# Kernel tuning notes

Hardware: AMD Instinct MI355X
Metric: run time of the kernel (lower is better)

## Reference

```python
import jax, jax.numpy as jnp
import numpy as np

B, T, C = 2, 2048, 2048
H, HD = 16, 128          # n_head, head_dim
LORA = C // 4            # kv_lora_rank = n_embd // compression_ratio
RD = HD // 2             # qk_rope_dim
ND = HD - RD             # qk_nope_dim
THETA = 100000.0


def setup_inputs() -> dict:
    key = jax.random.key(0)
    k0, k1, k2, k3, k4 = jax.random.split(key, 5)
    s = 0.02
    return {
        "x": jax.random.normal(k0, (B, T, C), dtype=jnp.float32),
        "Wq": jax.random.normal(k1, (C, H * HD), dtype=jnp.float32) * s,
        "Wkva": jax.random.normal(k2, (C, LORA + RD), dtype=jnp.float32) * s,
        "Wkvb": jax.random.normal(k3, (LORA, H * ND), dtype=jnp.float32) * s,
        "Wo": jax.random.normal(k4, (H * HD, C), dtype=jnp.float32) * s,
    }


def apply_rope(x, theta=THETA):
    # x: [B, H, T, D] with D even; interleaved complex rotation (torch.view_as_complex style)
    b, h, t, d = x.shape
    freqs = 1.0 / (theta ** (jnp.arange(0, d, 2, dtype=jnp.float32) / d))  # [D/2]
    ang = jnp.arange(t, dtype=jnp.float32)[:, None] * freqs[None, :]       # [T, D/2]
    cos, sin = jnp.cos(ang), jnp.sin(ang)
    xr = x.reshape(b, h, t, d // 2, 2)
    x0, x1 = xr[..., 0], xr[..., 1]
    o0 = x0 * cos - x1 * sin
    o1 = x0 * sin + x1 * cos
    return jnp.stack([o0, o1], axis=-1).reshape(b, h, t, d)


def reference(x, Wq, Wkva, Wkvb, Wo):
    Bx, Tx, Cx = x.shape
    # query projection -> [B, H, T, HD]
    q = (x @ Wq).reshape(Bx, Tx, H, HD).transpose(0, 2, 1, 3)
    # compressed KV + shared (MQA) rope key
    ckv = x @ Wkva                                  # [B, T, LORA+RD]
    kv_latent = ckv[..., :LORA]                     # [B, T, LORA]
    k_rope = ckv[..., LORA:]                        # [B, T, RD]
    # decompress nope part of K (== nope part of V)
    kv = (kv_latent @ Wkvb).reshape(Bx, Tx, H, ND).transpose(0, 2, 1, 3)  # [B,H,T,ND]
    k_rope = jnp.broadcast_to(k_rope[:, None, :, :], (Bx, H, Tx, RD))
    q_nope, q_rope = q[..., :ND], q[..., ND:]
    q_rope = apply_rope(q_rope)
    k_rope = apply_rope(k_rope)
    qf = jnp.concatenate([q_nope, q_rope], axis=-1)               # [B,H,T,HD]
    kf = jnp.concatenate([kv, k_rope], axis=-1)                   # [B,H,T,HD]
    vf = jnp.concatenate([kv, jnp.zeros_like(k_rope)], axis=-1)   # [B,H,T,HD]
    scale = 1.0 / np.sqrt(HD).astype(np.float32)
    att = jnp.einsum("bhtd,bhsd->bhts", qf, kf) * scale           # [B,H,T,T]
    causal = jnp.tril(jnp.ones((Tx, Tx), dtype=bool))
    att = jnp.where(causal, att, -jnp.inf)
    att = jax.nn.softmax(att, axis=-1)
    y = jnp.einsum("bhts,bhsd->bhtd", att, vf)                    # [B,H,T,HD]
    y = y.transpose(0, 2, 1, 3).reshape(Bx, Tx, H * HD)
    return y @ Wo
```

## Files before the change

kernel.cpp:

```cpp
#include <hip/hip_runtime.h>
#include <hip/hip_bf16.h>
#include <math.h>

#define B_ 2
#define T_ 2048
#define C_ 2048
#define H_ 16
#define HD_ 128
#define LORA_ 512
#define RD_ 64
#define ND_ 64
#define BT_ (B_*T_)
#define NKVA_ 576
#define NKVAP_ 640
#define LOG2_THETA 16.609640474436812f

typedef __bf16 bf16x8 __attribute__((ext_vector_type(8)));
typedef float  f32x4  __attribute__((ext_vector_type(4)));

#define MFMA16(a,b,c) __builtin_amdgcn_mfma_f32_16x16x32_bf16((a),(b),(c),0,0,0)

__device__ static inline void load_lds16(const __bf16* g, __bf16* l) {
  auto* lp = (__attribute__((address_space(3))) char*)(uintptr_t)(l);
  auto* gp = (const __attribute__((address_space(1))) char*)(g);
  __builtin_amdgcn_global_load_lds(gp, lp, 16, 0, 0);
}

__device__ static inline unsigned pkbf(float a, float b) {
  union { __bf16 h[2]; unsigned u; } v;
  v.h[0] = (__bf16)a; v.h[1] = (__bf16)b;
  return v.u;
}

__global__ __launch_bounds__(256) void k_cast_x(const float* __restrict__ x,
                                                __bf16* __restrict__ xb, int n) {
  int idx = blockIdx.x * 256 + threadIdx.x;
  if (idx < n) xb[idx] = (__bf16)x[idx];
}

__global__ __launch_bounds__(256) void k_tcast(const float* __restrict__ src,
                                               __bf16* __restrict__ dst,
                                               int K, int N, int NP) {
  __shared__ float tile[32][33];
  int k0 = blockIdx.x * 32;
  int n0 = blockIdx.y * 32;
  int tx = threadIdx.x & 31, ty = threadIdx.x >> 5;
  for (int i = ty; i < 32; i += 8) {
    int n = n0 + tx;
    tile[i][tx] = (n < N) ? src[(size_t)(k0 + i) * N + n] : 0.0f;
  }
  __syncthreads();
  for (int i = ty; i < 32; i += 8) {
    dst[(size_t)(n0 + i) * K + k0 + tx] = (__bf16)tile[tx][i];
  }
}

__global__ __launch_bounds__(256) void k_tcast_wo(const float* __restrict__ Wo,
                                                  __bf16* __restrict__ dst) {
  __shared__ float tile[32][33];
  int kc0 = blockIdx.x * 32;
  int n0  = blockIdx.y * 32;
  int rbase = (kc0 >> 6) * 128 + (kc0 & 63);
  int tx = threadIdx.x & 31, ty = threadIdx.x >> 5;
  for (int i = ty; i < 32; i += 8)
    tile[i][tx] = Wo[(size_t)(rbase + i) * C_ + n0 + tx];
  __syncthreads();
  for (int i = ty; i < 32; i += 8)
    dst[(size_t)(n0 + i) * 1024 + kc0 + tx] = (__bf16)tile[tx][i];
}

__global__ __launch_bounds__(256) void k_gemm_bt(const __bf16* __restrict__ A,
                                                 const __bf16* __restrict__ B,
                                                 float* __restrict__ C,
                                                 int M, int N, int K) {
  __shared__ __align__(16) __bf16 As[2][128 * 32];
  __shared__ __align__(16) __bf16 Bs[2][128 * 32];
  const int tid  = threadIdx.x;
  const int lane = tid & 63;
  const int wave = tid >> 6;
  const int bm = blockIdx.x, bn = blockIdx.y;
  const int r0 = tid >> 2;
  const int c8 = (tid & 3) * 8;
  const __bf16* Ag = A + (size_t)(bm * 128 + r0) * K + c8;
  const __bf16* Bg = B + (size_t)(bn * 128 + r0) * K + c8;
  const int wr = (wave >> 1) * 64, wc = (wave & 1) * 64;
  const int fr = lane & 15, fk = (lane >> 4) * 8;
  const f32x4 fzero = {0.f, 0.f, 0.f, 0.f};
  f32x4 acc[4][4];
#pragma unroll
  for (int i = 0; i < 4; ++i)
#pragma unroll
    for (int j = 0; j < 4; ++j) acc[i][j] = fzero;

  load_lds16(Ag,                  &As[0][tid * 8]);
  load_lds16(Ag + (size_t)64 * K, &As[0][tid * 8 + 2048]);
  load_lds16(Bg,                  &Bs[0][tid * 8]);
  load_lds16(Bg + (size_t)64 * K, &Bs[0][tid * 8 + 2048]);

  int buf = 0;
  for (int k0 = 0; k0 < K; k0 += 32) {
    __syncthreads();
    if (k0 + 32 < K) {
      const int nb = buf ^ 1;
      load_lds16(Ag + k0 + 32,                  &As[nb][tid * 8]);
      load_lds16(Ag + (size_t)64 * K + k0 + 32, &As[nb][tid * 8 + 2048]);
      load_lds16(Bg + k0 + 32,                  &Bs[nb][tid * 8]);
      load_lds16(Bg + (size_t)64 * K + k0 + 32, &Bs[nb][tid * 8 + 2048]);
    }
    bf16x8 af[4], bfg[4];
#pragma unroll
    for (int i = 0; i < 4; ++i) af[i]  = *(const bf16x8*)&As[buf][(wr + i * 16 + fr) * 32 + fk];
#pragma unroll
    for (int j = 0; j < 4; ++j) bfg[j] = *(const bf16x8*)&Bs[buf][(wc + j * 16 + fr) * 32 + fk];
#pragma unroll
    for (int i = 0; i < 4; ++i)
#pragma unroll
      for (int j = 0; j < 4; ++j)
        acc[i][j] = MFMA16(af[i], bfg[j], acc[i][j]);
    buf ^= 1;
  }
  const int rbase = (lane >> 4) * 4;
  float* Cb = C + (size_t)(bm * 128 + wr + rbase) * N + bn * 128 + wc + fr;
#pragma unroll
  for (int i = 0; i < 4; ++i)
#pragma unroll
    for (int j = 0; j < 4; ++j)
#pragma unroll
      for (int r = 0; r < 4; ++r)
        Cb[(size_t)(i * 16 + r) * N + j * 16] = acc[i][j][r];
}

__global__ __launch_bounds__(256) void k_rope_q(const float* __restrict__ q,
                                                __bf16* __restrict__ qf) {
  const float scale2 = 1.4426950408889634f / 11.313708498984760f;
  int idx = blockIdx.x * 256 + threadIdx.x;
  int d  = idx & 127;
  int t  = (idx >> 7) & 2047;
  int bh = idx >> 18;
  int h  = bh & 15, b = bh >> 4;
  const float* qrow = q + ((size_t)(b * T_ + t)) * 2048 + h * 128;
  float v;
  if (d < 64) {
    v = qrow[d];
  } else {
    int i = (d - 64) >> 1;
    float freq = exp2f(-((float)(2 * i) / 64.0f) * LOG2_THETA);
    float ang = (float)t * freq;
    float c = cosf(ang), s = sinf(ang);
    float x0 = qrow[64 + 2 * i], x1 = qrow[64 + 2 * i + 1];
    v = (d & 1) ? (x0 * s + x1 * c) : (x0 * c - x1 * s);
  }
  qf[idx] = (__bf16)(v * scale2);
}

__global__ __launch_bounds__(256) void k_rope_kf(const float* __restrict__ ckv,
                                                 __bf16* __restrict__ kf) {
  int idx = blockIdx.x * 256 + threadIdx.x;
  int d = idx & 63;
  int t = (idx >> 6) & 2047;
  int h = (idx >> 17) & 15;
  int b = idx >> 21;
  const float* src = ckv + ((size_t)(b * T_ + t)) * NKVAP_ + 512;
  int i = d >> 1;
  float freq = exp2f(-((float)(2 * i) / 64.0f) * LOG2_THETA);
  float ang = (float)t * freq;
  float c = cosf(ang), s = sinf(ang);
  float x0 = src[2 * i], x1 = src[2 * i + 1];
  float v = (d & 1) ? (x0 * s + x1 * c) : (x0 * c - x1 * s);
  kf[(((size_t)(b * H_ + h)) * T_ + t) * 128 + 64 + d] = (__bf16)v;
}

__global__ __launch_bounds__(256) void k_cast_kvl(const float* __restrict__ ckv,
                                                  __bf16* __restrict__ kvl) {
  int idx = blockIdx.x * 256 + threadIdx.x;
  int r = idx >> 9, c = idx & 511;
  kvl[idx] = (__bf16)ckv[(size_t)r * NKVAP_ + c];
}

__global__ __launch_bounds__(256) void k_pack_kv(const float* __restrict__ kv,
                                                 __bf16* __restrict__ kf,
                                                 __bf16* __restrict__ kvT) {
  __shared__ float tile[64][65];
  const int bh = blockIdx.x;
  const int b = bh >> 4, h = bh & 15;
  const int t0 = blockIdx.y * 64;
  const int tid = threadIdx.x;
  const int i0 = tid >> 4, d4 = (tid & 15) * 4;
#pragma unroll
  for (int p = 0; p < 4; ++p) {
    int i = i0 + p * 16;
    const float* src = kv + ((size_t)(b * T_ + t0 + i)) * 1024 + h * 64 + d4;
    float4 v = *(const float4*)src;
    tile[i][d4] = v.x; tile[i][d4 + 1] = v.y; tile[i][d4 + 2] = v.z; tile[i][d4 + 3] = v.w;
    union { __bf16 hh[4]; uint2 u; } o;
    o.hh[0] = (__bf16)v.x; o.hh[1] = (__bf16)v.y; o.hh[2] = (__bf16)v.z; o.hh[3] = (__bf16)v.w;
    *(uint2*)(kf + ((size_t)bh * T_ + t0 + i) * 128 + d4) = o.u;
  }
  __syncthreads();
  const int dd = tid >> 2, tc0 = (tid & 3) * 16;
  __bf16 outv[16];
#pragma unroll
  for (int j = 0; j < 16; ++j) outv[j] = (__bf16)tile[tc0 + j][dd];
  __bf16* dst = kvT + ((size_t)(bh * 64 + dd)) * T_ + t0 + tc0;
  *(bf16x8*)dst = *(bf16x8*)&outv[0];
  *(bf16x8*)(dst + 8) = *(bf16x8*)&outv[8];
}

__global__ __launch_bounds__(256, 3) void k_attn(const __bf16* __restrict__ qf,
                                                 const __bf16* __restrict__ kf,
                                                 const __bf16* __restrict__ kvT,
                                                 __bf16* __restrict__ yc) {
  const int blk = blockIdx.x;
  const int bh = blk & 31;
  const int qt = 31 - (blk >> 5);
  const int b = bh >> 4, h = bh & 15;
  const int qbase = qt * 64;
  const int tid = threadIdx.x;
  const int lane = tid & 63, wave = tid >> 6;
  const int fr = lane & 15, quad = lane >> 4, fk8 = quad * 8;

  __shared__ __align__(16) __bf16 Ks[2][64 * 128];
  __shared__ __align__(16) __bf16 Vs[2][64 * 64];

  const int qi = qbase + wave * 16 + fr;
  const __bf16* qb = qf + ((size_t)bh * T_ + qi) * HD_;
  bf16x8 aq[4];
#pragma unroll
  for (int g = 0; g < 4; ++g) aq[g] = *(const bf16x8*)(qb + g * 32 + fk8);

  const f32x4 fzero = {0.f, 0.f, 0.f, 0.f};
  f32x4 accO[4];
#pragma unroll
  for (int g = 0; g < 4; ++g) accO[g] = fzero;
  float m = -1e30f, l = 0.f;

  const int srow = tid >> 4, scolh = (tid & 15) * 8;
  const int vrow = tid >> 3, vcolh = (tid & 7) * 8;
  const int kwcol = scolh ^ ((srow & 7) * 8);
  const int vwcol = vcolh ^ ((vrow & 7) * 8);
  const int kswz = (fr & 7) * 8;
  const __bf16* kbh = kf + (size_t)bh * T_ * 128;
  const __bf16* vbh = kvT + (size_t)bh * 64 * T_;
  const int srcA = (quad & 1) * 32 + fr, srcB = srcA + 16;
  const int hi = quad >> 1;

  bf16x8 kreg[4], vreg[2];
  auto load_regs = [&](int S) {
#pragma unroll
    for (int p = 0; p < 4; ++p)
      kreg[p] = *(const bf16x8*)(kbh + (size_t)(S + srow + p * 16) * 128 + scolh);
#pragma unroll
    for (int p = 0; p < 2; ++p)
      vreg[p] = *(const bf16x8*)(vbh + (size_t)(vrow + p * 32) * T_ + S + vcolh);
  };
  auto write_buf = [&](int bufi) {
#pragma unroll
    for (int p = 0; p < 4; ++p)
      *(bf16x8*)&Ks[bufi][(srow + p * 16) * 128 + kwcol] = kreg[p];
#pragma unroll
    for (int p = 0; p < 2; ++p)
      *(bf16x8*)&Vs[bufi][(vrow + p * 32) * 64 + vwcol] = vreg[p];
  };

  load_regs(0);
  write_buf(0);
  if (qbase > 0) load_regs(64);
  __syncthreads();

  int cur = 0;
  for (int s0 = 0; s0 <= qbase; s0 += 64) {
    if (s0 + 64 <= qbase) write_buf(cur ^ 1);
    if (s0 + 128 <= qbase) load_regs(s0 + 128);

    f32x4 accST[4];
#pragma unroll
    for (int cg = 0; cg < 4; ++cg) accST[cg] = fzero;
    __builtin_amdgcn_s_setprio(1);
#pragma unroll
    for (int cg = 0; cg < 4; ++cg) {
#pragma unroll
      for (int kg = 0; kg < 4; ++kg) {
        bf16x8 bk = *(const bf16x8*)&Ks[cur][(cg * 16 + fr) * 128 + ((kg * 32 + fk8) ^ kswz)];
        accST[cg] = MFMA16(bk, aq[kg], accST[cg]);
      }
    }
    __builtin_amdgcn_s_setprio(0);

    float lmax = -1e30f;
    if (s0 == qbase) {
#pragma unroll
      for (int cg = 0; cg < 4; ++cg) {
#pragma unroll
        for (int r = 0; r < 4; ++r) {
          const int key = s0 + cg * 16 + quad * 4 + r;
          float v = accST[cg][r];
          v = (key <= qi) ? v : -1e30f;
          accST[cg][r] = v;
          lmax = fmaxf(lmax, v);
        }
      }
    } else {
#pragma unroll
      for (int cg = 0; cg < 4; ++cg) {
#pragma unroll
        for (int r = 0; r < 4; ++r) lmax = fmaxf(lmax, accST[cg][r]);
      }
    }
    lmax = fmaxf(lmax, __shfl_xor(lmax, 16, 64));
    lmax = fmaxf(lmax, __shfl_xor(lmax, 32, 64));

    if (!__all(lmax <= m + 8.0f)) {
      const float mn = fmaxf(m, lmax);
      const float alpha = exp2f(m - mn);
      l *= alpha;
#pragma unroll
      for (int g = 0; g < 4; ++g)
#pragma unroll
        for (int r = 0; r < 4; ++r) accO[g][r] *= alpha;
      m = mn;
    }

    float lsum = 0.f;
    unsigned pk0[4], pk1[4];
#pragma unroll
    for (int cg = 0; cg < 4; ++cg) {
      float p0 = exp2f(accST[cg][0] - m);
      float p1 = exp2f(accST[cg][1] - m);
      float p2 = exp2f(accST[cg][2] - m);
      float p3 = exp2f(accST[cg][3] - m);
      lsum += (p0 + p1) + (p2 + p3);
      pk0[cg] = pkbf(p0, p1);
      pk1[cg] = pkbf(p2, p3);
    }
    lsum += __shfl_xor(lsum, 16, 64);
    lsum += __shfl_xor(lsum, 32, 64);
    l += lsum;

#pragma unroll
    for (int ks = 0; ks < 2; ++ks) {
      int a0 = __shfl((int)pk0[2 * ks], srcA, 64);
      int b0 = __shfl((int)pk0[2 * ks + 1], srcA, 64);
      int a1 = __shfl((int)pk1[2 * ks], srcA, 64);
      int b1 = __shfl((int)pk1[2 * ks + 1], srcA, 64);
      int a2 = __shfl((int)pk0[2 * ks], srcB, 64);
      int b2 = __shfl((int)pk0[2 * ks + 1], srcB, 64);
      int a3 = __shfl((int)pk1[2 * ks], srcB, 64);
      int b3 = __shfl((int)pk1[2 * ks + 1], srcB, 64);
      union { int i[4]; bf16x8 v; } pf;
      pf.i[0] = hi ? b0 : a0;
      pf.i[1] = hi ? b1 : a1;
      pf.i[2] = hi ? b2 : a2;
      pf.i[3] = hi ? b3 : a3;
      __builtin_amdgcn_s_setprio(1);
#pragma unroll
      for (int g = 0; g < 4; ++g) {
        bf16x8 vv = *(const bf16x8*)&Vs[cur][(g * 16 + fr) * 64 + ((ks * 32 + fk8) ^ kswz)];
        accO[g] = MFMA16(vv, pf.v, accO[g]);
      }
      __builtin_amdgcn_s_setprio(0);
    }

    __syncthreads();
    cur ^= 1;
  }

  const float linv = 1.0f / l;
  __bf16* yb = yc + ((size_t)(b * T_ + qi)) * 1024 + h * 64 + quad * 4;
#pragma unroll
  for (int g = 0; g < 4; ++g) {
    union { unsigned u[2]; uint2 v; } o;
    o.u[0] = pkbf(accO[g][0] * linv, accO[g][1] * linv);
    o.u[1] = pkbf(accO[g][2] * linv, accO[g][3] * linv);
    *(uint2*)(yb + g * 16) = o.v;
  }
}

extern "C" void kernel_launch(void* const* d_in, const int* in_sizes, int n_in,
                              void* d_out, int out_size, void* d_ws, size_t ws_size,
                              hipStream_t stream) {
  const float* x    = (const float*)d_in[0];
  const float* Wq   = (const float*)d_in[1];
  const float* Wkva = (const float*)d_in[2];
  const float* Wkvb = (const float*)d_in[3];
  const float* Wo   = (const float*)d_in[4];
  float* out = (float*)d_out;
  char* ws = (char*)d_ws;

  size_t off = 0;
  __bf16* xb    = (__bf16*)(ws + off); off += (size_t)BT_ * C_ * 2;
  __bf16* WqT   = (__bf16*)(ws + off); off += (size_t)2048 * 2048 * 2;
  __bf16* WkvaT = (__bf16*)(ws + off); off += (size_t)NKVAP_ * 2048 * 2;
  __bf16* WkvbT = (__bf16*)(ws + off); off += (size_t)1024 * 512 * 2;
  __bf16* WoTc  = (__bf16*)(ws + off); off += (size_t)2048 * 1024 * 2;
  float*  q     = (float*)(ws + off);  off += (size_t)BT_ * 2048 * 4;
  float*  ckv   = (float*)(ws + off);  off += (size_t)BT_ * NKVAP_ * 4;
  __bf16* kvl   = (__bf16*)(ws + off); off += (size_t)BT_ * 512 * 2;
  float*  kv    = (float*)(ws + off);  off += (size_t)BT_ * 1024 * 4;
  __bf16* qfb   = (__bf16*)(ws + off); off += (size_t)B_ * H_ * T_ * HD_ * 2;
  __bf16* yc    = (__bf16*)(ws + off); off += (size_t)BT_ * 1024 * 2;
  __bf16* kfb = (__bf16*)q;
  __bf16* kvT = (__bf16*)((char*)q + (size_t)B_ * H_ * T_ * HD_ * 2);

  k_cast_x<<<(BT_ * C_) / 256, 256, 0, stream>>>(x, xb, BT_ * C_);
  k_tcast<<<dim3(2048 / 32, 2048 / 32), 256, 0, stream>>>(Wq, WqT, 2048, 2048, 2048);
  k_tcast<<<dim3(2048 / 32, NKVAP_ / 32), 256, 0, stream>>>(Wkva, WkvaT, 2048, NKVA_, NKVAP_);
  k_tcast<<<dim3(512 / 32, 1024 / 32), 256, 0, stream>>>(Wkvb, WkvbT, 512, 1024, 1024);
  k_tcast_wo<<<dim3(1024 / 32, 2048 / 32), 256, 0, stream>>>(Wo, WoTc);

  k_gemm_bt<<<dim3(BT_ / 128, 2048 / 128), 256, 0, stream>>>(xb, WqT, q, BT_, 2048, 2048);
  k_gemm_bt<<<dim3(BT_ / 128, NKVAP_ / 128), 256, 0, stream>>>(xb, WkvaT, ckv, BT_, NKVAP_, 2048);

  k_rope_q<<<(B_ * H_ * T_ * HD_) / 256, 256, 0, stream>>>(q, qfb);
  k_cast_kvl<<<(BT_ * 512) / 256, 256, 0, stream>>>(ckv, kvl);

  k_gemm_bt<<<dim3(BT_ / 128, 1024 / 128), 256, 0, stream>>>(kvl, WkvbT, kv, BT_, 1024, 512);
  k_pack_kv<<<dim3(B_ * H_, T_ / 64), 256, 0, stream>>>(kv, kfb, kvT);
  k_rope_kf<<<(B_ * H_ * T_ * 64) / 256, 256, 0, stream>>>(ckv, kfb);

  k_attn<<<(T_ / 64) * B_ * H_, 256, 0, stream>>>(qfb, kfb, kvT, yc);

  k_gemm_bt<<<dim3(BT_ / 128, 2048 / 128), 256, 0, stream>>>(yc, WoTc, out, BT_, 2048, 1024);
}
```

Baseline: 343.5 us.

## Process 128 query rows per attention block, two 16-row tiles per wave

The attention kernel now handles 128 queries per block (32 per wave as two 16-row MFMA tiles), so each K/V tile loaded into LDS is reused across twice as many queries and K/V fragment reads feed two MFMAs. Online softmax state is duplicated per sub-tile, and waves skip key tiles entirely past their causal limit. This halves grid size and raises register pressure (launch bounds lowered to 2 blocks/SIMD), trading occupancy and load balance for reduced K/V traffic.

```diff
diff --git a/kernel.cpp b/kernel.cpp
--- a/kernel.cpp
+++ b/kernel.cpp
@@ -206,15 +206,15 @@
   *(bf16x8*)(dst + 8) = *(bf16x8*)&outv[8];
 }
 
-__global__ __launch_bounds__(256, 3) void k_attn(const __bf16* __restrict__ qf,
+__global__ __launch_bounds__(256, 2) void k_attn(const __bf16* __restrict__ qf,
                                                  const __bf16* __restrict__ kf,
                                                  const __bf16* __restrict__ kvT,
                                                  __bf16* __restrict__ yc) {
   const int blk = blockIdx.x;
   const int bh = blk & 31;
-  const int qt = 31 - (blk >> 5);
+  const int qt = 15 - (blk >> 5);
   const int b = bh >> 4, h = bh & 15;
-  const int qbase = qt * 64;
+  const int qbase = qt * 128;
   const int tid = threadIdx.x;
   const int lane = tid & 63, wave = tid >> 6;
   const int fr = lane & 15, quad = lane >> 4, fk8 = quad * 8;
@@ -222,17 +222,20 @@
   __shared__ __align__(16) __bf16 Ks[2][64 * 128];
   __shared__ __align__(16) __bf16 Vs[2][64 * 64];
 
-  const int qi = qbase + wave * 16 + fr;
-  const __bf16* qb = qf + ((size_t)bh * T_ + qi) * HD_;
-  bf16x8 aq[4];
-#pragma unroll
-  for (int g = 0; g < 4; ++g) aq[g] = *(const bf16x8*)(qb + g * 32 + fk8);
+  const int qw = qbase + wave * 32;
+  bf16x8 aq[2][4];
+#pragma unroll
+  for (int jq = 0; jq < 2; ++jq) {
+    const __bf16* qb = qf + ((size_t)bh * T_ + qw + jq * 16 + fr) * HD_;
+#pragma unroll
+    for (int g = 0; g < 4; ++g) aq[jq][g] = *(const bf16x8*)(qb + g * 32 + fk8);
+  }
 
   const f32x4 fzero = {0.f, 0.f, 0.f, 0.f};
-  f32x4 accO[4];
-#pragma unroll
-  for (int g = 0; g < 4; ++g) accO[g] = fzero;
-  float m = -1e30f, l = 0.f;
+  f32x4 accO[4][2];
+#pragma unroll
+  for (int g = 0; g < 4; ++g) { accO[g][0] = fzero; accO[g][1] = fzero; }
+  float m0 = -1e30f, m1 = -1e30f, l0 = 0.f, l1 = 0.f;
 
   const int srow = tid >> 4, scolh = (tid & 15) * 8;
   const int vrow = tid >> 3, vcolh = (tid & 7) * 8;
@@ -261,117 +264,146 @@
     for (int p = 0; p < 2; ++p)
       *(bf16x8*)&Vs[bufi][(vrow + p * 32) * 64 + vwcol] = vreg[p];
   };
-
+  auto build_pf = [&](const unsigned* pk0, const unsigned* pk1, int ks) {
+    int a0 = __shfl((int)pk0[2 * ks], srcA, 64);
+    int b0 = __shfl((int)pk0[2 * ks + 1], srcA, 64);
+    int a1 = __shfl((int)pk1[2 * ks], srcA, 64);
+    int b1 = __shfl((int)pk1[2 * ks + 1], srcA, 64);
+    int a2 = __shfl((int)pk0[2 * ks], srcB, 64);
+    int b2 = __shfl((int)pk0[2 * ks + 1], srcB, 64);
+    int a3 = __shfl((int)pk1[2 * ks], srcB, 64);
+    int b3 = __shfl((int)pk1[2 * ks + 1], srcB, 64);
+    union { int i[4]; bf16x8 v; } pf;
+    pf.i[0] = hi ? b0 : a0;
+    pf.i[1] = hi ? b1 : a1;
+    pf.i[2] = hi ? b2 : a2;
+    pf.i[3] = hi ? b3 : a3;
+    return pf.v;
+  };
+
+  const int smax = qbase + 64;
   load_regs(0);
   write_buf(0);
-  if (qbase > 0) load_regs(64);
+  load_regs(64);
   __syncthreads();
 
   int cur = 0;
-  for (int s0 = 0; s0 <= qbase; s0 += 64) {
-    if (s0 + 64 <= qbase) write_buf(cur ^ 1);
-    if (s0 + 128 <= qbase) load_regs(s0 + 128);
-
-    f32x4 accST[4];
-#pragma unroll
-    for (int cg = 0; cg < 4; ++cg) accST[cg] = fzero;
-    __builtin_amdgcn_s_setprio(1);
-#pragma unroll
-    for (int cg = 0; cg < 4; ++cg) {
-#pragma unroll
-      for (int kg = 0; kg < 4; ++kg) {
-        bf16x8 bk = *(const bf16x8*)&Ks[cur][(cg * 16 + fr) * 128 + ((kg * 32 + fk8) ^ kswz)];
-        accST[cg] = MFMA16(bk, aq[kg], accST[cg]);
+  for (int s0 = 0; s0 <= smax; s0 += 64) {
+    if (s0 + 64 <= smax) write_buf(cur ^ 1);
+    if (s0 + 128 <= smax) load_regs(s0 + 128);
+
+    if (s0 <= qw + 31) {
+      f32x4 accST[4][2];
+#pragma unroll
+      for (int cg = 0; cg < 4; ++cg) { accST[cg][0] = fzero; accST[cg][1] = fzero; }
+      __builtin_amdgcn_s_setprio(1);
+#pragma unroll
+      for (int cg = 0; cg < 4; ++cg) {
+#pragma unroll
+        for (int kg = 0; kg < 4; ++kg) {
+          bf16x8 bk = *(const bf16x8*)&Ks[cur][(cg * 16 + fr) * 128 + ((kg * 32 + fk8) ^ kswz)];
+          accST[cg][0] = MFMA16(bk, aq[0][kg], accST[cg][0]);
+          accST[cg][1] = MFMA16(bk, aq[1][kg], accST[cg][1]);
+        }
+      }
+      __builtin_amdgcn_s_setprio(0);
+
+      float lmax0 = -1e30f, lmax1 = -1e30f;
+      if (s0 + 63 > qw) {
+        const int qi0 = qw + fr, qi1 = qw + 16 + fr;
+#pragma unroll
+        for (int cg = 0; cg < 4; ++cg) {
+#pragma unroll
+          for (int r = 0; r < 4; ++r) {
+            const int key = s0 + cg * 16 + quad * 4 + r;
+            float v0 = accST[cg][0][r], v1 = accST[cg][1][r];
+            v0 = (key <= qi0) ? v0 : -1e30f;
+            v1 = (key <= qi1) ? v1 : -1e30f;
+            accST[cg][0][r] = v0; accST[cg][1][r] = v1;
+            lmax0 = fmaxf(lmax0, v0); lmax1 = fmaxf(lmax1, v1);
+          }
+        }
+      } else {
+#pragma unroll
+        for (int cg = 0; cg < 4; ++cg) {
+#pragma unroll
+          for (int r = 0; r < 4; ++r) {
+            lmax0 = fmaxf(lmax0, accST[cg][0][r]);
+            lmax1 = fmaxf(lmax1, accST[cg][1][r]);
+          }
+        }
+      }
+      lmax0 = fmaxf(lmax0, __shfl_xor(lmax0, 16, 64));
+      lmax0 = fmaxf(lmax0, __shfl_xor(lmax0, 32, 64));
+      lmax1 = fmaxf(lmax1, __shfl_xor(lmax1, 16, 64));
+      lmax1 = fmaxf(lmax1, __shfl_xor(lmax1, 32, 64));
+
+      if (!__all(lmax0 <= m0 + 8.0f && lmax1 <= m1 + 8.0f)) {
+        const float mn0 = fmaxf(m0, lmax0), mn1 = fmaxf(m1, lmax1);
+        const float al0 = exp2f(m0 - mn0), al1 = exp2f(m1 - mn1);
+        l0 *= al0; l1 *= al1;
+#pragma unroll
+        for (int g = 0; g < 4; ++g) {
+#pragma unroll
+          for (int r = 0; r < 4; ++r) { accO[g][0][r] *= al0; accO[g][1][r] *= al1; }
+        }
+        m0 = mn0; m1 = mn1;
+      }
+
+      float ls0 = 0.f, ls1 = 0.f;
+      unsigned pk0a[4], pk1a[4], pk0b[4], pk1b[4];
+#pragma unroll
+      for (int cg = 0; cg < 4; ++cg) {
+        float p0 = exp2f(accST[cg][0][0] - m0);
+        float p1 = exp2f(accST[cg][0][1] - m0);
+        float p2 = exp2f(accST[cg][0][2] - m0);
+        float p3 = exp2f(accST[cg][0][3] - m0);
+        ls0 += (p0 + p1) + (p2 + p3);
+        pk0a[cg] = pkbf(p0, p1); pk1a[cg] = pkbf(p2, p3);
+        float r0 = exp2f(accST[cg][1][0] - m1);
+        float r1 = exp2f(accST[cg][1][1] - m1);
+        float r2 = exp2f(accST[cg][1][2] - m1);
+        float r3 = exp2f(accST[cg][1][3] - m1);
+        ls1 += (r0 + r1) + (r2 + r3);
+        pk0b[cg] = pkbf(r0, r1); pk1b[cg] = pkbf(r2, r3);
+      }
+      ls0 += __shfl_xor(ls0, 16, 64);
+      ls0 += __shfl_xor(ls0, 32, 64);
+      ls1 += __shfl_xor(ls1, 16, 64);
+      ls1 += __shfl_xor(ls1, 32, 64);
+      l0 += ls0; l1 += ls1;
+
+#pragma unroll
+      for (int ks = 0; ks < 2; ++ks) {
+        bf16x8 pfa = build_pf(pk0a, pk1a, ks);
+        bf16x8 pfb = build_pf(pk0b, pk1b, ks);
+        __builtin_amdgcn_s_setprio(1);
+#pragma unroll
+        for (int g = 0; g < 4; ++g) {
+          bf16x8 vv = *(const bf16x8*)&Vs[cur][(g * 16 + fr) * 64 + ((ks * 32 + fk8) ^ kswz)];
+          accO[g][0] = MFMA16(vv, pfa, accO[g][0]);
+          accO[g][1] = MFMA16(vv, pfb, accO[g][1]);
+        }
+        __builtin_amdgcn_s_setprio(0);
       }
     }
-    __builtin_amdgcn_s_setprio(0);
-
-    float lmax = -1e30f;
-    if (s0 == qbase) {
-#pragma unroll
-      for (int cg = 0; cg < 4; ++cg) {
-#pragma unroll
-        for (int r = 0; r < 4; ++r) {
-          const int key = s0 + cg * 16 + quad * 4 + r;
-          float v = accST[cg][r];
-          v = (key <= qi) ? v : -1e30f;
-          accST[cg][r] = v;
-          lmax = fmaxf(lmax, v);
-        }
-      }
-    } else {
-#pragma unroll
-      for (int cg = 0; cg < 4; ++cg) {
-#pragma unroll
-        for (int r = 0; r < 4; ++r) lmax = fmaxf(lmax, accST[cg][r]);
-      }
-    }
-    lmax = fmaxf(lmax, __shfl_xor(lmax, 16, 64));
-    lmax = fmaxf(lmax, __shfl_xor(lmax, 32, 64));
-
-    if (!__all(lmax <= m + 8.0f)) {
-      const float mn = fmaxf(m, lmax);
-      const float alpha = exp2f(m - mn);
-      l *= alpha;
-#pragma unroll
-      for (int g = 0; g < 4; ++g)
-#pragma unroll
-        for (int r = 0; r < 4; ++r) accO[g][r] *= alpha;
-      m = mn;
-    }
-
-    float lsum = 0.f;
-    unsigned pk0[4], pk1[4];
-#pragma unroll
-    for (int cg = 0; cg < 4; ++cg) {
-      float p0 = exp2f(accST[cg][0] - m);
-      float p1 = exp2f(accST[cg][1] - m);
-      float p2 = exp2f(accST[cg][2] - m);
-      float p3 = exp2f(accST[cg][3] - m);
-      lsum += (p0 + p1) + (p2 + p3);
-      pk0[cg] = pkbf(p0, p1);
-      pk1[cg] = pkbf(p2, p3);
-    }
-    lsum += __shfl_xor(lsum, 16, 64);
-    lsum += __shfl_xor(lsum, 32, 64);
-    l += lsum;
-
-#pragma unroll
-    for (int ks = 0; ks < 2; ++ks) {
-      int a0 = __shfl((int)pk0[2 * ks], srcA, 64);
-      int b0 = __shfl((int)pk0[2 * ks + 1], srcA, 64);
-      int a1 = __shfl((int)pk1[2 * ks], srcA, 64);
-      int b1 = __shfl((int)pk1[2 * ks + 1], srcA, 64);
-      int a2 = __shfl((int)pk0[2 * ks], srcB, 64);
-      int b2 = __shfl((int)pk0[2 * ks + 1], srcB, 64);
-      int a3 = __shfl((int)pk1[2 * ks], srcB, 64);
-      int b3 = __shfl((int)pk1[2 * ks + 1], srcB, 64);
-      union { int i[4]; bf16x8 v; } pf;
-      pf.i[0] = hi ? b0 : a0;
-      pf.i[1] = hi ? b1 : a1;
-      pf.i[2] = hi ? b2 : a2;
-      pf.i[3] = hi ? b3 : a3;
-      __builtin_amdgcn_s_setprio(1);
-#pragma unroll
-      for (int g = 0; g < 4; ++g) {
-        bf16x8 vv = *(const bf16x8*)&Vs[cur][(g * 16 + fr) * 64 + ((ks * 32 + fk8) ^ kswz)];
-        accO[g] = MFMA16(vv, pf.v, accO[g]);
-      }
-      __builtin_amdgcn_s_setprio(0);
-    }
 
     __syncthreads();
     cur ^= 1;
   }
 
-  const float linv = 1.0f / l;
-  __bf16* yb = yc + ((size_t)(b * T_ + qi)) * 1024 + h * 64 + quad * 4;
+  const float li0 = 1.0f / l0, li1 = 1.0f / l1;
+  __bf16* yb0 = yc + ((size_t)(b * T_ + qw + fr)) * 1024 + h * 64 + quad * 4;
+  __bf16* yb1 = yc + ((size_t)(b * T_ + qw + 16 + fr)) * 1024 + h * 64 + quad * 4;
 #pragma unroll
   for (int g = 0; g < 4; ++g) {
     union { unsigned u[2]; uint2 v; } o;
-    o.u[0] = pkbf(accO[g][0] * linv, accO[g][1] * linv);
-    o.u[1] = pkbf(accO[g][2] * linv, accO[g][3] * linv);
-    *(uint2*)(yb + g * 16) = o.v;
+    o.u[0] = pkbf(accO[g][0][0] * li0, accO[g][0][1] * li0);
+    o.u[1] = pkbf(accO[g][0][2] * li0, accO[g][0][3] * li0);
+    *(uint2*)(yb0 + g * 16) = o.v;
+    o.u[0] = pkbf(accO[g][1][0] * li1, accO[g][1][1] * li1);
+    o.u[1] = pkbf(accO[g][1][2] * li1, accO[g][1][3] * li1);
+    *(uint2*)(yb1 + g * 16) = o.v;
   }
 }
 
@@ -417,7 +449,7 @@
   k_pack_kv<<<dim3(B_ * H_, T_ / 64), 256, 0, stream>>>(kv, kfb, kvT);
   k_rope_kf<<<(B_ * H_ * T_ * 64) / 256, 256, 0, stream>>>(ckv, kfb);
 
-  k_attn<<<(T_ / 64) * B_ * H_, 256, 0, stream>>>(qfb, kfb, kvT, yc);
+  k_attn<<<(T_ / 128) * B_ * H_, 256, 0, stream>>>(qfb, kfb, kvT, yc);
 
   k_gemm_bt<<<dim3(BT_ / 128, 2048 / 128), 256, 0, stream>>>(yc, WoTc, out, BT_, 2048, 1024);
 }
```

Measured after the change: 358.6 us. 4.4% more time.
